# Kernel tuning notes

Hardware: AMD Instinct MI355X
Metric: run time of the kernel (lower is better)

The kernel has to match this reference:

```python
import jax, jax.numpy as jnp
import numpy as np

D_MODEL = 768
NUM_HEADS = 12
D_K = D_MODEL // NUM_HEADS


def setup_inputs() -> dict:
    key = jax.random.key(0)
    ks = jax.random.split(key, 9)
    B, S = 2, 4096
    s = 1.0 / np.sqrt(D_MODEL).astype(np.float32)
    inp = {
        "x": jax.random.normal(ks[0], (B, S, D_MODEL), dtype=jnp.float32),
        "wq": jax.random.normal(ks[1], (D_MODEL, D_MODEL), dtype=jnp.float32) * s,
        "bq": jnp.zeros((D_MODEL,), dtype=jnp.float32),
        "wk": jax.random.normal(ks[2], (D_MODEL, D_MODEL), dtype=jnp.float32) * s,
        "bk": jnp.zeros((D_MODEL,), dtype=jnp.float32),
        "wv": jax.random.normal(ks[3], (D_MODEL, D_MODEL), dtype=jnp.float32) * s,
        "bv": jnp.zeros((D_MODEL,), dtype=jnp.float32),
        "wo": jax.random.normal(ks[4], (D_MODEL, D_MODEL), dtype=jnp.float32) * s,
        "bo": jnp.zeros((D_MODEL,), dtype=jnp.float32),
    }
    return inp


def reference(x, wq, bq, wk, bk, wv, bv, wo, bo):
    B, S, D = x.shape
    H, dk = NUM_HEADS, D_K
    # projections (torch Linear: x @ W^T + b); weights here stored as [in, out]
    def proj(w, b):
        y = jnp.einsum("bsd,df->bsf", x, w) + b
        return y.reshape(B, S, H, dk).transpose(0, 2, 1, 3)  # [B,H,S,dk]
    q = proj(wq, bq)
    k = proj(wk, bk)
    v = proj(wv, bv)
    scores = jnp.einsum("bhqd,bhkd->bhqk", q, k) / np.sqrt(dk).astype(np.float32)
    attn = jax.nn.softmax(scores, axis=-1)  # dropout is identity in eval
    out = jnp.einsum("bhqk,bhkd->bhqd", attn, v)
    out = out.transpose(0, 2, 1, 3).reshape(B, S, D)
    return jnp.einsum("bsd,df->bsf", out, wo) + bo
```

## Files before the change

kernel.cpp:

```cpp
#include <hip/hip_runtime.h>

typedef unsigned short u16;
typedef unsigned int u32;
typedef __bf16 bf16x8 __attribute__((ext_vector_type(8)));
typedef short s16x4 __attribute__((ext_vector_type(4)));
typedef float f32x4 __attribute__((ext_vector_type(4)));

#define AS1(p) ((const __attribute__((address_space(1))) void*)(p))
#define AS3(p) ((__attribute__((address_space(3))) void*)(p))

#if __has_builtin(__builtin_amdgcn_exp2f)
#define EXP2(x) __builtin_amdgcn_exp2f(x)
#else
#define EXP2(x) __builtin_exp2f(x)
#endif

__device__ __forceinline__ u16 f2bf(float f) {
    u32 u = __float_as_uint(f);
    u += 0x7fffu + ((u >> 16) & 1u);
    return (u16)(u >> 16);
}

__device__ __forceinline__ short bfbits(float f) {
    __bf16 h = (__bf16)f;
    return __builtin_bit_cast(short, h);
}

#define NXQ 6291456
#define QSCALE 0.1803368801111249f

__global__ __launch_bounds__(256) void prep_kernel(
    const float* __restrict__ x,
    const float* __restrict__ wq, const float* __restrict__ wk,
    const float* __restrict__ wv, const float* __restrict__ wo,
    const float* __restrict__ bq, const float* __restrict__ bk,
    const float* __restrict__ bv,
    u16* __restrict__ xbf, u16* __restrict__ WT, float* __restrict__ bqkv)
{
    const int t = threadIdx.x;
    const int bid = blockIdx.x;
    if (bid < 6144) {
        int i = bid * 256 + t;
        float4 v = ((const float4*)x)[i];
        uint2 o;
        o.x = (u32)f2bf(v.x) | ((u32)f2bf(v.y) << 16);
        o.y = (u32)f2bf(v.z) | ((u32)f2bf(v.w) << 16);
        ((uint2*)xbf)[i] = o;
        return;
    }
    int tb = bid - 6144;
    int mat = tb / 144;
    int tt = tb - mat * 144;
    int tr = tt / 12, tc = tt - tr * 12;
    const float* W = (mat == 0) ? wq : (mat == 1) ? wk : (mat == 2) ? wv : wo;
    __shared__ u16 sT[64 * 72];
    #pragma unroll
    for (int rr = 0; rr < 4; ++rr) {
        int r = (t >> 4) + rr * 16;
        int cb = (t & 15) * 4;
        float4 v = *(const float4*)&W[(size_t)(tr * 64 + r) * 768 + tc * 64 + cb];
        sT[(cb + 0) * 72 + r] = f2bf(v.x);
        sT[(cb + 1) * 72 + r] = f2bf(v.y);
        sT[(cb + 2) * 72 + r] = f2bf(v.z);
        sT[(cb + 3) * 72 + r] = f2bf(v.w);
    }
    __syncthreads();
    #pragma unroll
    for (int i = 0; i < 2; ++i) {
        int nr = t >> 2;
        int cc = (t & 3) * 16 + i * 8;
        *(uint4*)&WT[(size_t)(mat * 768 + tc * 64 + nr) * 768 + tr * 64 + cc] =
            *(uint4*)&sT[nr * 72 + cc];
    }
    if (tb < 9) {
        int i = tb * 256 + t;
        if (i < 2304)
            bqkv[i] = (i < 768) ? bq[i] : (i < 1536) ? bk[i - 768] : bv[i - 1536];
    }
}

__global__ __launch_bounds__(256, 4) void gemm_qkv(
    const u16* __restrict__ A, const u16* __restrict__ WT,
    const float* __restrict__ bias, u16* __restrict__ out)
{
    __shared__ u16 sA[2][128 * 32];
    __shared__ u16 sB[2][128 * 32];
    const int m0 = blockIdx.x * 128;
    const int n0g = blockIdx.y * 128;
    const int tid = threadIdx.x, lane = tid & 63, wave = tid >> 6;
    const int quad = lane >> 4, l16 = lane & 15;
    const int wm = (wave & 1) * 64, wn = (wave >> 1) * 64;

    f32x4 acc[4][4];
    #pragma unroll
    for (int i = 0; i < 4; ++i)
        #pragma unroll
        for (int j = 0; j < 4; ++j)
            #pragma unroll
            for (int r = 0; r < 4; ++r)
                acc[i][j][r] = 0.f;

    const int srow = lane >> 2;
    const int scc = lane & 3;

    auto stage = [&](int k0, int buf) {
        #pragma unroll
        for (int i = 0; i < 2; ++i) {
            int c = wave * 2 + i;
            int row = c * 16 + srow;
            int kc = (scc ^ (row & 3)) * 8;
            __builtin_amdgcn_global_load_lds(
                AS1(&A[(size_t)(m0 + row) * 768 + k0 + kc]),
                AS3(&sA[buf][c * 512]), 16, 0, 0);
            __builtin_amdgcn_global_load_lds(
                AS1(&WT[(size_t)(n0g + row) * 768 + k0 + kc]),
                AS3(&sB[buf][c * 512]), 16, 0, 0);
        }
    };

    auto compute = [&](int buf) {
        bf16x8 af[4], bfr[4];
        #pragma unroll
        for (int i = 0; i < 4; ++i) {
            int row = wm + i * 16 + l16;
            af[i] = *(const bf16x8*)&sA[buf][row * 32 + ((quad ^ (row & 3)) * 8)];
        }
        #pragma unroll
        for (int j = 0; j < 4; ++j) {
            int row = wn + j * 16 + l16;
            bfr[j] = *(const bf16x8*)&sB[buf][row * 32 + ((quad ^ (row & 3)) * 8)];
        }
        #pragma unroll
        for (int i = 0; i < 4; ++i)
            #pragma unroll
            for (int j = 0; j < 4; ++j)
                acc[i][j] = __builtin_amdgcn_mfma_f32_16x16x32_bf16(af[i], bfr[j], acc[i][j], 0, 0, 0);
    };

    stage(0, 0);
    for (int kt = 0; kt < 24; kt += 2) {
        __syncthreads();
        stage((kt + 1) * 32, 1);
        compute(0);
        __syncthreads();
        if (kt + 2 < 24) stage((kt + 2) * 32, 0);
        compute(1);
    }

    const int mat = blockIdx.y / 6;
    const int nm0 = n0g - mat * 768;
    const float scale = (mat == 0) ? QSCALE : 1.0f;
    u16* dst = out + (size_t)mat * NXQ;
    #pragma unroll
    for (int i = 0; i < 4; ++i) {
        #pragma unroll
        for (int j = 0; j < 4; ++j) {
            int colg = n0g + wn + j * 16 + l16;
            int col = nm0 + wn + j * 16 + l16;
            float bv = bias[colg];
            int h = col >> 6, d = col & 63;
            int row0 = m0 + wm + i * 16 + quad * 4;
            int b = row0 >> 12, s = row0 & 4095;
            if (mat < 2) {
                #pragma unroll
                for (int r = 0; r < 4; ++r)
                    dst[(((size_t)(b * 12 + h) * 4096) + s + r) * 64 + d] =
                        f2bf((acc[i][j][r] + bv) * scale);
            } else {
                ushort4 w;
                w.x = f2bf(acc[i][j][0] + bv);
                w.y = f2bf(acc[i][j][1] + bv);
                w.z = f2bf(acc[i][j][2] + bv);
                w.w = f2bf(acc[i][j][3] + bv);
                *(ushort4*)&dst[(((size_t)(b * 12 + h) * 64 + d) * 4096) + s] = w;
            }
        }
    }
}

__global__ __launch_bounds__(256, 4) void gemm_out(
    const u16* __restrict__ A, const u16* __restrict__ WT,
    const float* __restrict__ bias, float* __restrict__ out)
{
    __shared__ u16 sA[2][64 * 32];
    __shared__ u16 sB[2][128 * 32];
    const int m0 = blockIdx.x * 64;
    const int n0 = blockIdx.y * 128;
    const int tid = threadIdx.x, lane = tid & 63, wave = tid >> 6;
    const int quad = lane >> 4, l16 = lane & 15;
    const int wm = (wave & 1) * 32, wn = (wave >> 1) * 64;

    f32x4 acc[2][4];
    #pragma unroll
    for (int i = 0; i < 2; ++i)
        #pragma unroll
        for (int j = 0; j < 4; ++j)
            #pragma unroll
            for (int r = 0; r < 4; ++r)
                acc[i][j][r] = 0.f;

    const int srow = lane >> 2;
    const int scc = lane & 3;

    auto stage = [&](int k0, int buf) {
        {
            int row = wave * 16 + srow;
            int kc = (scc ^ (row & 3)) * 8;
            __builtin_amdgcn_global_load_lds(
                AS1(&A[(size_t)(m0 + row) * 768 + k0 + kc]),
                AS3(&sA[buf][wave * 512]), 16, 0, 0);
        }
        #pragma unroll
        for (int i = 0; i < 2; ++i) {
            int c = wave * 2 + i;
            int row = c * 16 + srow;
            int kc = (scc ^ (row & 3)) * 8;
            __builtin_amdgcn_global_load_lds(
                AS1(&WT[(size_t)(n0 + row) * 768 + k0 + kc]),
                AS3(&sB[buf][c * 512]), 16, 0, 0);
        }
    };

    auto compute = [&](int buf) {
        bf16x8 af[2], bfr[4];
        #pragma unroll
        for (int i = 0; i < 2; ++i) {
            int row = wm + i * 16 + l16;
            af[i] = *(const bf16x8*)&sA[buf][row * 32 + ((quad ^ (row & 3)) * 8)];
        }
        #pragma unroll
        for (int j = 0; j < 4; ++j) {
            int row = wn + j * 16 + l16;
            bfr[j] = *(const bf16x8*)&sB[buf][row * 32 + ((quad ^ (row & 3)) * 8)];
        }
        #pragma unroll
        for (int i = 0; i < 2; ++i)
            #pragma unroll
            for (int j = 0; j < 4; ++j)
                acc[i][j] = __builtin_amdgcn_mfma_f32_16x16x32_bf16(af[i], bfr[j], acc[i][j], 0, 0, 0);
    };

    stage(0, 0);
    for (int kt = 0; kt < 24; kt += 2) {
        __syncthreads();
        stage((kt + 1) * 32, 1);
        compute(0);
        __syncthreads();
        if (kt + 2 < 24) stage((kt + 2) * 32, 0);
        compute(1);
    }

    #pragma unroll
    for (int i = 0; i < 2; ++i) {
        #pragma unroll
        for (int j = 0; j < 4; ++j) {
            int col = n0 + wn + j * 16 + l16;
            float bv = bias[col];
            #pragma unroll
            for (int r = 0; r < 4; ++r) {
                int row = m0 + wm + i * 16 + quad * 4 + r;
                out[(size_t)row * 768 + col] = acc[i][j][r] + bv;
            }
        }
    }
}

__global__ __launch_bounds__(256, 2) void flash_kernel(
    const u16* __restrict__ Q, const u16* __restrict__ K,
    const u16* __restrict__ Vt, u16* __restrict__ O)
{
    const int bh = blockIdx.y;
    const int q0 = blockIdx.x * 128;
    const u16* Qp = Q + (size_t)bh * 4096 * 64;
    const u16* Kp = K + (size_t)bh * 4096 * 64;
    const u16* Vp = Vt + (size_t)bh * 64 * 4096;
    const int tid = threadIdx.x, lane = tid & 63, wave = tid >> 6;
    const int quad = lane >> 4, l16 = lane & 15;

    __shared__ u16 sK[2][64 * 64];
    __shared__ u16 sVT[2][64 * 64];

    const int qrow = q0 + wave * 32;
    bf16x8 qf[2][2];
    #pragma unroll
    for (int i = 0; i < 2; ++i)
        #pragma unroll
        for (int s = 0; s < 2; ++s)
            qf[i][s] = *(const bf16x8*)&Qp[(size_t)(qrow + i * 16 + l16) * 64 + s * 32 + quad * 8];

    f32x4 oacc[4][2];
    f32x4 lacc[2];
    #pragma unroll
    for (int jd = 0; jd < 4; ++jd)
        #pragma unroll
        for (int i = 0; i < 2; ++i)
            #pragma unroll
            for (int r = 0; r < 4; ++r)
                oacc[jd][i][r] = 0.f;
    #pragma unroll
    for (int i = 0; i < 2; ++i)
        #pragma unroll
        for (int r = 0; r < 4; ++r)
            lacc[i][r] = 0.f;

    s16x4 ones;
    #pragma unroll
    for (int r = 0; r < 4; ++r) ones[r] = (short)0x3F80;

    const int srow = lane >> 3;
    auto stage = [&](int t, int buf) {
        #pragma unroll
        for (int i = 0; i < 2; ++i) {
            int c = wave * 2 + i;
            int row = c * 8 + srow;
            int kc = ((lane & 7) ^ (row & 7)) * 8;
            __builtin_amdgcn_global_load_lds(
                AS1(&Kp[(size_t)(t * 64 + row) * 64 + kc]),
                AS3(&sK[buf][c * 512]), 16, 0, 0);
            __builtin_amdgcn_global_load_lds(
                AS1(&Vp[(size_t)row * 4096 + t * 64 + kc]),
                AS3(&sVT[buf][c * 512]), 16, 0, 0);
        }
    };

    auto body = [&](int cur) {
        f32x4 sacc[4][2];
        #pragma unroll
        for (int m = 0; m < 4; ++m)
            #pragma unroll
            for (int i = 0; i < 2; ++i)
                #pragma unroll
                for (int r = 0; r < 4; ++r)
                    sacc[m][i][r] = 0.f;
        #pragma unroll
        for (int s = 0; s < 2; ++s) {
            bf16x8 ak[4];
            #pragma unroll
            for (int m = 0; m < 4; ++m) {
                int row = m * 16 + l16;
                ak[m] = *(const bf16x8*)&sK[cur][row * 64 + (((s * 4 + quad) ^ (row & 7)) * 8)];
            }
            #pragma unroll
            for (int m = 0; m < 4; ++m)
                #pragma unroll
                for (int i = 0; i < 2; ++i)
                    sacc[m][i] = __builtin_amdgcn_mfma_f32_16x16x32_bf16(ak[m], qf[i][s], sacc[m][i], 0, 0, 0);
        }

        s16x4 bp[4][2];
        #pragma unroll
        for (int i = 0; i < 2; ++i) {
            #pragma unroll
            for (int kk = 0; kk < 4; ++kk) {
                s16x4 b;
                b[0] = bfbits(EXP2(sacc[kk][i][0]));
                b[1] = bfbits(EXP2(sacc[kk][i][1]));
                b[2] = bfbits(EXP2(sacc[kk][i][2]));
                b[3] = bfbits(EXP2(sacc[kk][i][3]));
                bp[kk][i] = b;
            }
        }

        #pragma unroll
        for (int kk = 0; kk < 4; ++kk) {
            s16x4 av[4];
            #pragma unroll
            for (int jd = 0; jd < 4; ++jd) {
                int row = jd * 16 + l16;
                av[jd] = *(const s16x4*)&sVT[cur][row * 64 +
                            (((kk * 2 + (quad >> 1)) ^ (row & 7)) * 8) + (quad & 1) * 4];
            }
            #pragma unroll
            for (int i = 0; i < 2; ++i) {
                #pragma unroll
                for (int jd = 0; jd < 4; ++jd)
                    oacc[jd][i] = __builtin_amdgcn_mfma_f32_16x16x16bf16_1k(av[jd], bp[kk][i], oacc[jd][i], 0, 0, 0);
                lacc[i] = __builtin_amdgcn_mfma_f32_16x16x16bf16_1k(ones, bp[kk][i], lacc[i], 0, 0, 0);
            }
        }
    };

    stage(0, 0);
    for (int t = 0; t < 64; t += 2) {
        __syncthreads();
        stage(t + 1, 1);
        body(0);
        __syncthreads();
        if (t + 2 < 64) stage(t + 2, 0);
        body(1);
    }

    const int b = bh / 12, h = bh - b * 12;
    #pragma unroll
    for (int i = 0; i < 2; ++i) {
        float inv = 1.0f / lacc[i][0];
        int s = qrow + i * 16 + l16;
        #pragma unroll
        for (int jd = 0; jd < 4; ++jd) {
            ushort4 w;
            w.x = f2bf(oacc[jd][i][0] * inv);
            w.y = f2bf(oacc[jd][i][1] * inv);
            w.z = f2bf(oacc[jd][i][2] * inv);
            w.w = f2bf(oacc[jd][i][3] * inv);
            *(ushort4*)&O[((size_t)(b * 4096 + s)) * 768 + h * 64 + jd * 16 + quad * 4] = w;
        }
    }
}

extern "C" void kernel_launch(void* const* d_in, const int* in_sizes, int n_in,
                              void* d_out, int out_size, void* d_ws, size_t ws_size,
                              hipStream_t stream)
{
    (void)in_sizes; (void)n_in; (void)out_size; (void)ws_size;
    const float* x  = (const float*)d_in[0];
    const float* wq = (const float*)d_in[1];
    const float* bq = (const float*)d_in[2];
    const float* wk = (const float*)d_in[3];
    const float* bk = (const float*)d_in[4];
    const float* wv = (const float*)d_in[5];
    const float* bv = (const float*)d_in[6];
    const float* wo = (const float*)d_in[7];
    const float* bo = (const float*)d_in[8];
    float* out = (float*)d_out;

    u16* ws = (u16*)d_ws;
    u16* xbf = ws;
    u16* WT  = xbf + (size_t)8192 * 768;
    u16* Qb  = WT + (size_t)3072 * 768;
    u16* Kb  = Qb + NXQ;
    u16* Vtb = Kb + NXQ;
    u16* Ob  = Vtb + NXQ;
    float* bqkv = (float*)(Ob + NXQ);

    prep_kernel<<<6720, 256, 0, stream>>>(x, wq, wk, wv, wo, bq, bk, bv, xbf, WT, bqkv);
    gemm_qkv<<<dim3(64, 18), 256, 0, stream>>>(xbf, WT, bqkv, Qb);
    flash_kernel<<<dim3(32, 24), 256, 0, stream>>>(Qb, Kb, Vtb, Ob);
    gemm_out<<<dim3(128, 6), 256, 0, stream>>>(Ob, WT + (size_t)2304 * 768, bo, out);
}
```

Measured before the change: 286.4 us.

## Fuse x fp32-to-bf16 conversion into QKV GEMM and stage epilogue via LDS

Drops the separate pass that converts x to bf16 in prep_kernel. gemm_qkv now loads fp32 x directly, converts it in registers and writes it to LDS, which removes one full round-trip of x through global memory. The epilogue now stages the output tile in shared memory so that Q/K and transposed V are written with coalesced 16-byte stores instead of scattered 2-byte stores. The cost is more fp32 global traffic on the A operand, since x is re-read across 18 column blocks. The A staging also loses its async global-to-LDS path and now needs extra synchronisation.

```diff
diff --git a/kernel.cpp b/kernel.cpp
--- a/kernel.cpp
+++ b/kernel.cpp
@@ -30,25 +30,14 @@
 #define QSCALE 0.1803368801111249f
 
 __global__ __launch_bounds__(256) void prep_kernel(
-    const float* __restrict__ x,
     const float* __restrict__ wq, const float* __restrict__ wk,
     const float* __restrict__ wv, const float* __restrict__ wo,
     const float* __restrict__ bq, const float* __restrict__ bk,
     const float* __restrict__ bv,
-    u16* __restrict__ xbf, u16* __restrict__ WT, float* __restrict__ bqkv)
+    u16* __restrict__ WT, float* __restrict__ bqkv)
 {
     const int t = threadIdx.x;
-    const int bid = blockIdx.x;
-    if (bid < 6144) {
-        int i = bid * 256 + t;
-        float4 v = ((const float4*)x)[i];
-        uint2 o;
-        o.x = (u32)f2bf(v.x) | ((u32)f2bf(v.y) << 16);
-        o.y = (u32)f2bf(v.z) | ((u32)f2bf(v.w) << 16);
-        ((uint2*)xbf)[i] = o;
-        return;
-    }
-    int tb = bid - 6144;
+    const int tb = blockIdx.x;
     int mat = tb / 144;
     int tt = tb - mat * 144;
     int tr = tt / 12, tc = tt - tr * 12;
@@ -80,11 +69,10 @@
 }
 
 __global__ __launch_bounds__(256, 4) void gemm_qkv(
-    const u16* __restrict__ A, const u16* __restrict__ WT,
+    const float* __restrict__ X, const u16* __restrict__ WT,
     const float* __restrict__ bias, u16* __restrict__ out)
 {
-    __shared__ u16 sA[2][128 * 32];
-    __shared__ u16 sB[2][128 * 32];
+    __shared__ u16 sh[16384];
     const int m0 = blockIdx.x * 128;
     const int n0g = blockIdx.y * 128;
     const int tid = threadIdx.x, lane = tid & 63, wave = tid >> 6;
@@ -103,18 +91,32 @@
     const int srow = lane >> 2;
     const int scc = lane & 3;
 
-    auto stage = [&](int k0, int buf) {
+    auto stageA = [&](int k0, int buf) {
+        #pragma unroll
+        for (int i = 0; i < 2; ++i) {
+            int c = wave * 2 + i;
+            int row = c * 16 + srow;
+            int kc = (scc ^ (row & 3)) * 8;
+            const float* src = &X[(size_t)(m0 + row) * 768 + k0 + kc];
+            float4 v0 = *(const float4*)src;
+            float4 v1 = *(const float4*)(src + 4);
+            uint4 o;
+            o.x = (u32)f2bf(v0.x) | ((u32)f2bf(v0.y) << 16);
+            o.y = (u32)f2bf(v0.z) | ((u32)f2bf(v0.w) << 16);
+            o.z = (u32)f2bf(v1.x) | ((u32)f2bf(v1.y) << 16);
+            o.w = (u32)f2bf(v1.z) | ((u32)f2bf(v1.w) << 16);
+            *(uint4*)&sh[buf * 4096 + c * 512 + lane * 8] = o;
+        }
+    };
+    auto stageB = [&](int k0, int buf) {
         #pragma unroll
         for (int i = 0; i < 2; ++i) {
             int c = wave * 2 + i;
             int row = c * 16 + srow;
             int kc = (scc ^ (row & 3)) * 8;
             __builtin_amdgcn_global_load_lds(
-                AS1(&A[(size_t)(m0 + row) * 768 + k0 + kc]),
-                AS3(&sA[buf][c * 512]), 16, 0, 0);
-            __builtin_amdgcn_global_load_lds(
                 AS1(&WT[(size_t)(n0g + row) * 768 + k0 + kc]),
-                AS3(&sB[buf][c * 512]), 16, 0, 0);
+                AS3(&sh[8192 + buf * 4096 + c * 512]), 16, 0, 0);
         }
     };
 
@@ -123,12 +125,12 @@
         #pragma unroll
         for (int i = 0; i < 4; ++i) {
             int row = wm + i * 16 + l16;
-            af[i] = *(const bf16x8*)&sA[buf][row * 32 + ((quad ^ (row & 3)) * 8)];
+            af[i] = *(const bf16x8*)&sh[buf * 4096 + row * 32 + ((quad ^ (row & 3)) * 8)];
         }
         #pragma unroll
         for (int j = 0; j < 4; ++j) {
             int row = wn + j * 16 + l16;
-            bfr[j] = *(const bf16x8*)&sB[buf][row * 32 + ((quad ^ (row & 3)) * 8)];
+            bfr[j] = *(const bf16x8*)&sh[8192 + buf * 4096 + row * 32 + ((quad ^ (row & 3)) * 8)];
         }
         #pragma unroll
         for (int i = 0; i < 4; ++i)
@@ -137,45 +139,54 @@
                 acc[i][j] = __builtin_amdgcn_mfma_f32_16x16x32_bf16(af[i], bfr[j], acc[i][j], 0, 0, 0);
     };
 
-    stage(0, 0);
+    stageB(0, 0); stageA(0, 0);
     for (int kt = 0; kt < 24; kt += 2) {
         __syncthreads();
-        stage((kt + 1) * 32, 1);
+        stageB((kt + 1) * 32, 1); stageA((kt + 1) * 32, 1);
         compute(0);
         __syncthreads();
-        if (kt + 2 < 24) stage((kt + 2) * 32, 0);
+        if (kt + 2 < 24) { stageB((kt + 2) * 32, 0); stageA((kt + 2) * 32, 0); }
         compute(1);
     }
 
+    __syncthreads();
     const int mat = blockIdx.y / 6;
     const int nm0 = n0g - mat * 768;
     const float scale = (mat == 0) ? QSCALE : 1.0f;
+    #pragma unroll
+    for (int i = 0; i < 4; ++i) {
+        #pragma unroll
+        for (int j = 0; j < 4; ++j) {
+            int col = wn + j * 16 + l16;
+            float bv = bias[n0g + col];
+            #pragma unroll
+            for (int r = 0; r < 4; ++r) {
+                int row = wm + i * 16 + quad * 4 + r;
+                u16 v = f2bf((acc[i][j][r] + bv) * scale);
+                if (mat < 2) sh[row * 128 + col] = v;
+                else         sh[col * 128 + row] = v;
+            }
+        }
+    }
+    __syncthreads();
+    const int r0 = tid >> 1, half = tid & 1;
     u16* dst = out + (size_t)mat * NXQ;
-    #pragma unroll
-    for (int i = 0; i < 4; ++i) {
-        #pragma unroll
-        for (int j = 0; j < 4; ++j) {
-            int colg = n0g + wn + j * 16 + l16;
-            int col = nm0 + wn + j * 16 + l16;
-            float bv = bias[colg];
-            int h = col >> 6, d = col & 63;
-            int row0 = m0 + wm + i * 16 + quad * 4;
-            int b = row0 >> 12, s = row0 & 4095;
-            if (mat < 2) {
-                #pragma unroll
-                for (int r = 0; r < 4; ++r)
-                    dst[(((size_t)(b * 12 + h) * 4096) + s + r) * 64 + d] =
-                        f2bf((acc[i][j][r] + bv) * scale);
-            } else {
-                ushort4 w;
-                w.x = f2bf(acc[i][j][0] + bv);
-                w.y = f2bf(acc[i][j][1] + bv);
-                w.z = f2bf(acc[i][j][2] + bv);
-                w.w = f2bf(acc[i][j][3] + bv);
-                *(ushort4*)&dst[(((size_t)(b * 12 + h) * 64 + d) * 4096) + s] = w;
-            }
-        }
-    }
+    u16* p;
+    if (mat < 2) {
+        int gs = m0 + r0;
+        int b = gs >> 12, s = gs & 4095;
+        int h = (nm0 + half * 64) >> 6;
+        p = &dst[(((size_t)(b * 12 + h) * 4096) + s) * 64];
+    } else {
+        int gd = nm0 + r0;
+        int h = gd >> 6, d = gd & 63;
+        int s0 = m0 + half * 64;
+        int b = s0 >> 12, s = s0 & 4095;
+        p = &dst[(((size_t)(b * 12 + h) * 64 + d) * 4096) + s];
+    }
+    #pragma unroll
+    for (int q = 0; q < 8; ++q)
+        *(uint4*)&p[q * 8] = *(uint4*)&sh[r0 * 128 + half * 64 + q * 8];
 }
 
 __global__ __launch_bounds__(256, 4) void gemm_out(
@@ -424,16 +435,15 @@
     float* out = (float*)d_out;
 
     u16* ws = (u16*)d_ws;
-    u16* xbf = ws;
-    u16* WT  = xbf + (size_t)8192 * 768;
+    u16* WT  = ws;
     u16* Qb  = WT + (size_t)3072 * 768;
     u16* Kb  = Qb + NXQ;
     u16* Vtb = Kb + NXQ;
     u16* Ob  = Vtb + NXQ;
     float* bqkv = (float*)(Ob + NXQ);
 
-    prep_kernel<<<6720, 256, 0, stream>>>(x, wq, wk, wv, wo, bq, bk, bv, xbf, WT, bqkv);
-    gemm_qkv<<<dim3(64, 18), 256, 0, stream>>>(xbf, WT, bqkv, Qb);
+    prep_kernel<<<576, 256, 0, stream>>>(wq, wk, wv, wo, bq, bk, bv, WT, bqkv);
+    gemm_qkv<<<dim3(64, 18), 256, 0, stream>>>(x, WT, bqkv, Qb);
     flash_kernel<<<dim3(32, 24), 256, 0, stream>>>(Qb, Kb, Vtb, Ob);
     gemm_out<<<dim3(128, 6), 256, 0, stream>>>(Ob, WT + (size_t)2304 * 768, bo, out);
 }
```

Result: slower. 313.8 us (+9.5%).
